# Optimization experiments

Hardware: AMD Instinct MI355X
Metric: run time of the kernel (lower is better)

The kernel has to match this reference:

```python
import jax, jax.numpy as jnp
import numpy as np

B, S, H, DH, D, FD, FU = 4, 256, 12, 64, 768, 2048, 2048


def setup_inputs() -> dict:
    key = jax.random.key(0)
    ks = jax.random.split(key, 12)
    s = 0.02  # typical init scale for weights
    return {
        "resid_pre": jax.random.normal(ks[0], (B, S, D), jnp.float32),
        "ln_scale": jax.random.uniform(ks[1], (B, S, 1), jnp.float32, 0.5, 2.0),
        "probs": jax.nn.softmax(jax.random.normal(ks[2], (B, H, S, S), jnp.float32), axis=-1),
        "W_O": jax.random.normal(ks[3], (H, DH, D), jnp.float32) * s,
        "W_V": jax.random.normal(ks[4], (H, D, DH), jnp.float32) * s,
        "enc_W": jax.random.normal(ks[5], (FD, D), jnp.float32) * s,
        "enc_b": jax.random.normal(ks[6], (FD,), jnp.float32) * s,
        "b_dec": jax.random.normal(ks[7], (D,), jnp.float32) * s,
        "up_dec_W": jax.random.normal(ks[8], (D, FU), jnp.float32) * s,
        "up_b_dec": jax.random.normal(ks[9], (D,), jnp.float32) * s,
        "pruned_features": jax.random.normal(ks[10], (B, S, FU), jnp.float32),
        "connection_mask": jax.random.randint(ks[11], (FD, FU), 0, 2, jnp.int32),
    }


def reference(resid_pre, ln_scale, probs, W_O, W_V, enc_W, enc_b, b_dec,
              up_dec_W, up_b_dec, pruned_features, connection_mask):
    # W_OV: [h, d_model(in), d_model(out)]
    W_OV = jnp.einsum('hko,hmk->hmo', W_O, W_V)
    mask = connection_mask.astype(resid_pre.dtype)

    # --- initial contributions ---
    act_ln = resid_pre / ln_scale                                  # [b,s,d]
    pre_moving = jnp.einsum('bsi,hio,fo->bshf', act_ln, W_OV, enc_W)  # [b,s,h,f_down]
    approx = jnp.einsum('bhqk,bkhf->bqf', probs, pre_moving)       # [b,q,f_down]

    # --- pruned contributions (one upstream AE) ---
    virtual = jnp.einsum('fo,hio,iu->hfu', enc_W, W_OV, up_dec_W) * mask[None]
    up_ln = pruned_features / ln_scale                             # [b,k,f_up]
    post_ov = jnp.einsum('bku,hfu->bhkf', up_ln, virtual)          # [b,h,k,f_down]
    approx = approx + jnp.einsum('bhqk,bhkf->bqf', probs, post_ov)

    # --- bias terms ---
    approx = approx + enc_b[None, None] - (enc_W @ b_dec)[None, None]
    ub_ln = up_b_dec[None, None] / ln_scale                        # [b,s,d]
    ub_post = jnp.einsum('hmd,bsm->bsd', W_OV, ub_ln)              # attn path through OV
    approx = approx + jnp.einsum('fd,bsd->bsf', enc_W, ub_post)
    return approx
```

## Files before the change

### kernel.cpp

```cpp
#include <hip/hip_runtime.h>
#include <hip/hip_bf16.h>
#include <stdint.h>

typedef __bf16 bf16;
typedef __bf16 bf16x8 __attribute__((ext_vector_type(8)));
typedef __bf16 bf16x4 __attribute__((ext_vector_type(4)));
typedef float f32x4 __attribute__((ext_vector_type(4)));

#define AS1 __attribute__((address_space(1)))
#define AS3 __attribute__((address_space(3)))


__device__ __forceinline__ void gld16(const bf16* g, bf16* l) {
  __builtin_amdgcn_global_load_lds((AS1 void*)g, (AS3 void*)l, 16, 0, 0);
}

__global__ void k_sentinel(float* __restrict__ out) {
  int i = blockIdx.x * 256 + threadIdx.x;
  if (i < 2097152) out[i] = 1048576.0f;
}


__global__ void k_invln(const float* __restrict__ ln, float* __restrict__ invln) {
  int i = blockIdx.x * 256 + threadIdx.x;
  if (i < 1024) invln[i] = 1.0f / ln[i];
}

__global__ void k_cast4(const float* __restrict__ s, bf16* __restrict__ d, int n4) {
  int i = blockIdx.x * 256 + threadIdx.x;
  if (i < n4) {
    float4 v = *(const float4*)(s + (long)i * 4);
    bf16x4 o;
    o[0] = (bf16)v.x; o[1] = (bf16)v.y; o[2] = (bf16)v.z; o[3] = (bf16)v.w;
    *(bf16x4*)(d + (long)i * 4) = o;
  }
}

__global__ void k_maskb(const int* __restrict__ m, bf16* __restrict__ d, int n4) {
  int i = blockIdx.x * 256 + threadIdx.x;
  if (i < n4) {
    int4 v = *(const int4*)(m + (long)i * 4);
    bf16x4 o;
    o[0] = (bf16)(float)v.x; o[1] = (bf16)(float)v.y;
    o[2] = (bf16)(float)v.z; o[3] = (bf16)(float)v.w;
    *(bf16x4*)(d + (long)i * 4) = o;
  }
}

__global__ void k_probsT(const float* __restrict__ probs, bf16* __restrict__ pT) {
  int i = blockIdx.x * 256 + threadIdx.x;
  if (i < 786432) {
    long idx = (long)i * 4;
    int s  = (int)(idx & 255);
    int q  = (int)((idx >> 8) & 255);
    int hb = (int)(idx >> 16);
    int h = hb % 12, b = hb / 12;
    float4 v = *(const float4*)(probs + idx);
    bf16x4 o;
    o[0] = (bf16)v.x; o[1] = (bf16)v.y; o[2] = (bf16)v.z; o[3] = (bf16)v.w;
    *(bf16x4*)(pT + (long)b * 786432 + (long)q * 3072 + h * 256 + s) = o;
  }
}

__global__ void k_WO(const float* __restrict__ W_O, bf16* __restrict__ WOb) {
  int i = blockIdx.x * 256 + threadIdx.x;
  int o = i % 768, r = (i / 768) & 127, h = i / (768 * 128);
  WOb[i] = (r < 64) ? (bf16)W_O[(long)(h * 64 + r) * 768 + o] : (bf16)0.0f;
}

__global__ void k_WVtT(const float* __restrict__ wv, bf16* __restrict__ WVt) {
  __shared__ float tile[32][33];
  int h = blockIdx.z;
  int k0 = blockIdx.x * 32;
  int i0 = blockIdx.y * 32;
  int lane = threadIdx.x & 31, rg = threadIdx.x >> 5;
  if (k0 < 64) {
    for (int r = rg; r < 32; r += 8)
      tile[r][lane] = wv[((long)(h * 768 + i0 + r)) * 64 + k0 + lane];
    __syncthreads();
    for (int r = rg; r < 32; r += 8)
      WVt[((long)h * 128 + k0 + r) * 768 + i0 + lane] = (bf16)tile[lane][r];
  } else {
    for (int r = rg; r < 32; r += 8)
      WVt[((long)h * 128 + k0 + r) * 768 + i0 + lane] = (bf16)0.0f;
  }
}

__global__ void k_WOt(const float* __restrict__ wo, bf16* __restrict__ W_Ot) {
  __shared__ float tile[32][33];
  int h = blockIdx.z;
  int k0 = blockIdx.x * 32;
  int o0 = blockIdx.y * 32;
  int lane = threadIdx.x & 31, rg = threadIdx.x >> 5;
  for (int r = rg; r < 32; r += 8)
    tile[r][lane] = wo[((long)(h * 64 + k0 + r)) * 768 + o0 + lane];
  __syncthreads();
  for (int r = rg; r < 32; r += 8)
    W_Ot[((long)(h * 768 + o0 + r)) * 64 + k0 + lane] = (bf16)tile[lane][r];
}

__global__ void k_updWtT(const float* __restrict__ u, bf16* __restrict__ d) {
  __shared__ float tile[32][33];
  int u0 = blockIdx.x * 32;
  int i0 = blockIdx.y * 32;
  int lane = threadIdx.x & 31, rg = threadIdx.x >> 5;
  for (int r = rg; r < 32; r += 8)
    tile[r][lane] = u[((long)(i0 + r)) * 2048 + u0 + lane];
  __syncthreads();
  for (int r = rg; r < 32; r += 8)
    d[((long)(u0 + r)) * 768 + i0 + lane] = (bf16)tile[lane][r];
}

__global__ void k_Xb(const float* __restrict__ resid, const float* __restrict__ invln,
                     bf16* __restrict__ Xb) {
  int i = blockIdx.x * 256 + threadIdx.x;
  if (i < 196608) {
    long idx = (long)i * 4;
    float il = invln[idx / 768];
    float4 v = *(const float4*)(resid + idx);
    bf16x4 o;
    o[0] = (bf16)(v.x * il); o[1] = (bf16)(v.y * il);
    o[2] = (bf16)(v.z * il); o[3] = (bf16)(v.w * il);
    *(bf16x4*)(Xb + idx) = o;
  }
}

__global__ void k_UtT(const float* __restrict__ pr, const float* __restrict__ invln,
                      bf16* __restrict__ Ut) {
  __shared__ float tile[32][33];
  int b = blockIdx.z, u0 = blockIdx.x * 32, s0 = blockIdx.y * 32;
  int lane = threadIdx.x & 31, rg = threadIdx.x >> 5;
  for (int r = rg; r < 32; r += 8) {
    int s = s0 + r;
    tile[r][lane] = pr[((long)(b * 256 + s)) * 2048 + u0 + lane] * invln[b * 256 + s];
  }
  __syncthreads();
  for (int r = rg; r < 32; r += 8)
    Ut[((long)b * 2048 + u0 + r) * 256 + s0 + lane] = (bf16)tile[lane][r];
}

__global__ void k_append(const bf16* __restrict__ encWb, bf16* __restrict__ Bt, long ldb) {
  int i = blockIdx.x * 256 + threadIdx.x;
  if (i < 196608) {
    long idx = (long)i * 8;
    int f = (int)(idx / 768), d = (int)(idx % 768);
    *(bf16x8*)(Bt + (long)f * ldb + d) = *(const bf16x8*)(encWb + idx);
  }
}


__device__ __forceinline__ float blk_reduce(float s) {
  __shared__ float red[256];
  red[threadIdx.x] = s; __syncthreads();
  for (int o = 128; o > 0; o >>= 1) {
    if ((int)threadIdx.x < o) red[threadIdx.x] += red[threadIdx.x + o];
    __syncthreads();
  }
  float r = red[0]; __syncthreads();
  return r;
}

__global__ void k_bias_t(const float* __restrict__ W_V, const float* __restrict__ up_b,
                         float* __restrict__ t_hk) {
  int j = blockIdx.x, h = j >> 6, k = j & 63;
  float s = 0.f;
  for (int m = threadIdx.x; m < 768; m += 256)
    s += W_V[((long)(h * 768 + m)) * 64 + k] * up_b[m];
  float r = blk_reduce(s);
  if (threadIdx.x == 0) t_hk[j] = r;
}

__global__ void k_bias_w(const float* __restrict__ W_O, const float* __restrict__ t_hk,
                         float* __restrict__ w) {
  int d = blockIdx.x;
  float s = 0.f;
  for (int j = threadIdx.x; j < 768; j += 256)
    s += W_O[(long)j * 768 + d] * t_hk[j];
  float r = blk_reduce(s);
  if (threadIdx.x == 0) w[d] = r;
}

__global__ void k_bias_c(const float* __restrict__ enc_W, const float* __restrict__ enc_b,
                         const float* __restrict__ b_dec, const float* __restrict__ w,
                         float* __restrict__ c0, float* __restrict__ c1) {
  int f = blockIdx.x;
  float s0 = 0.f, s1 = 0.f;
  for (int d = threadIdx.x; d < 768; d += 256) {
    float e = enc_W[(long)f * 768 + d];
    s0 += e * b_dec[d];
    s1 += e * w[d];
  }
  float r0 = blk_reduce(s0);
  float r1 = blk_reduce(s1);
  if (threadIdx.x == 0) { c0[f] = enc_b[f] - r0; c1[f] = r1; }
}

__global__ __launch_bounds__(256)
void gemm_bt(const bf16* __restrict__ A, const bf16* __restrict__ B, void* __restrict__ Cv,
             int M, int N, int K,
             long lda, long ldb, long ldc,
             int batchH,
             long sa_b, long sa_h, long sb_b, long sb_h, long sc_b, long sc_h,
             int mode, int kChunk,
             const bf16* __restrict__ mask, long mask_ld)
{
  __shared__ __align__(16) bf16 Asm[128 * 64];
  __shared__ __align__(16) bf16 Bsm[128 * 64];

  const int t = threadIdx.x;

  const int nbx = gridDim.x, nby = gridDim.y;
  const int nxy = nbx * nby;
  int orig = blockIdx.x + nbx * blockIdx.y;
  int qq = nxy >> 3, rr = nxy & 7;
  int xcd = orig & 7, lid = orig >> 3;
  int swz = (xcd < rr) ? (xcd * (qq + 1) + lid)
                       : (rr * (qq + 1) + (xcd - rr) * qq + lid);
  const int m0 = (swz % nby) * 128;
  const int n0 = (swz / nby) * 128;

  long aoff, boff, coff;
  int k0, k1;
  if (mode >= 2) {
    int z = blockIdx.z;
    aoff = 0; boff = 0;
    coff = (long)z * (long)M * ldc;
    k0 = z * kChunk; k1 = k0 + kChunk; if (k1 > K) k1 = K;
  } else {
    int z = blockIdx.z;
    int bb = z / batchH, hh = z - bb * batchH;
    aoff = (long)bb * sa_b + (long)hh * sa_h;
    boff = (long)bb * sb_b + (long)hh * sb_h;
    coff = (long)bb * sc_b + (long)hh * sc_h;
    k0 = 0; k1 = K;
  }

  const bf16* Ab = A + aoff + (long)m0 * lda;
  const bf16* Bb = B + boff + (long)n0 * ldb;

  const int r0 = t >> 3;
  const int g8 = t & 7;

  const int L = t & 63, w = t >> 6;
  const int wm = (w & 1) * 64, wn = (w >> 1) * 64;
  const int r16 = L & 15, q = L >> 4;

  f32x4 acc[4][4];
#pragma unroll
  for (int i = 0; i < 4; i++)
#pragma unroll
    for (int j = 0; j < 4; j++) acc[i][j] = (f32x4){0.f, 0.f, 0.f, 0.f};

  for (int kt = k0; kt < k1; kt += 64) {
#pragma unroll
    for (int j = 0; j < 4; j++) {
      int row = j * 32 + r0;
      int sc = ((g8 ^ (row & 7)) << 3);
      gld16(Ab + (long)row * lda + (kt + sc), &Asm[j * 2048 + t * 8]);
      gld16(Bb + (long)row * ldb + (kt + sc), &Bsm[j * 2048 + t * 8]);
    }
    __syncthreads();

#pragma unroll
    for (int h2 = 0; h2 < 2; h2++) {
      bf16x8 af[4], bfr[4];
#pragma unroll
      for (int i = 0; i < 4; i++) {
        int ra = wm + i * 16 + r16;
        af[i]  = *(const bf16x8*)&Asm[ra * 64 + ((((h2 << 2) + q) ^ (ra & 7)) << 3)];
        int rb = wn + i * 16 + r16;
        bfr[i] = *(const bf16x8*)&Bsm[rb * 64 + ((((h2 << 2) + q) ^ (rb & 7)) << 3)];
      }
#pragma unroll
      for (int mi = 0; mi < 4; mi++)
#pragma unroll
        for (int ni = 0; ni < 4; ni++)
          acc[mi][ni] = __builtin_amdgcn_mfma_f32_16x16x32_bf16(af[mi], bfr[ni], acc[mi][ni], 0, 0, 0);
    }
    __syncthreads();
  }

  if (mode >= 2) {
    float* C = (float*)Cv;
#pragma unroll
    for (int mi = 0; mi < 4; mi++)
#pragma unroll
      for (int ni = 0; ni < 4; ni++)
#pragma unroll
        for (int r = 0; r < 4; r++) {
          int gm = m0 + wm + mi * 16 + q * 4 + r;
          int gn = n0 + wn + ni * 16 + r16;
          long idx = coff + (long)gm * ldc + gn;
          float v = acc[mi][ni][r];
          if (mode == 3) v += C[idx];
          C[idx] = v;
        }
  } else {
    bf16* C = (bf16*)Cv;
#pragma unroll
    for (int mi = 0; mi < 4; mi++)
#pragma unroll
      for (int ni = 0; ni < 4; ni++)
#pragma unroll
        for (int r = 0; r < 4; r++) {
          int gm = m0 + wm + mi * 16 + q * 4 + r;
          int gn = n0 + wn + ni * 16 + r16;
          float v = acc[mi][ni][r];
          if (mode == 1) v *= (float)mask[(long)gm * mask_ld + gn];
          C[coff + (long)gm * ldc + gn] = (bf16)v;
        }
  }
}

__global__ __launch_bounds__(512, 2)
void gemm_fp2(const bf16* __restrict__ A, const bf16* __restrict__ B,
              float* __restrict__ C,
              int M, int N, int K, long lda, long ldb, long ldc,
              int mode, int kChunk)
{
  __shared__ __align__(16) bf16 SM[2][2][16384];

  const int t = threadIdx.x;

  const int nz = gridDim.z;
  int fid = blockIdx.x + gridDim.x * (blockIdx.y + gridDim.y * blockIdx.z);
  const int z  = fid % nz;
  const int t2 = fid / nz;
  const int m0 = (t2 >> 3) * 256;
  const int n0 = (t2 & 7) * 256;

  const long coff = (long)z * (long)M * ldc;
  int k0 = z * kChunk, k1 = k0 + kChunk; if (k1 > K) k1 = K;
  const int NT = (k1 > k0) ? (k1 - k0) >> 6 : 0;

  const bf16* Ab = A + (long)m0 * lda + k0;
  const bf16* Bb = B + (long)n0 * ldb + k0;

  const int sr = t >> 3;
  const int g8 = t & 7;

  const int L = t & 63, w = t >> 6;
  const int wm = (w & 1) * 128;
  const int wn = (w >> 1) * 64;
  const int r16 = L & 15, q = L >> 4;

  f32x4 acc[8][4];
#pragma unroll
  for (int i = 0; i < 8; i++)
#pragma unroll
    for (int j = 0; j < 4; j++) acc[i][j] = (f32x4){0.f, 0.f, 0.f, 0.f};

  auto stage = [&](int tt, int buf) {
    const bf16* Ap = Ab + (long)tt * 64;
    const bf16* Bp = Bb + (long)tt * 64;
#pragma unroll
    for (int j = 0; j < 4; j++) {
      int row = j * 64 + sr;
      int sc = ((g8 ^ (row & 7)) << 3);
      gld16(Ap + (long)row * lda + sc, &SM[buf][0][j * 4096 + t * 8]);
    }
#pragma unroll
    for (int j = 0; j < 4; j++) {
      int row = j * 64 + sr;
      int sc = ((g8 ^ (row & 7)) << 3);
      gld16(Bp + (long)row * ldb + sc, &SM[buf][1][j * 4096 + t * 8]);
    }
  };

  if (NT >= 1) stage(0, 0);

  for (int tt = 0; tt < NT; tt++) {
    if (tt + 1 < NT) {
      stage(tt + 1, (tt + 1) & 1);
      asm volatile("s_waitcnt vmcnt(8)" ::: "memory");
    } else {
      asm volatile("s_waitcnt vmcnt(0)" ::: "memory");
    }
    __builtin_amdgcn_s_barrier();

    const bf16* As = &SM[tt & 1][0][0];
    const bf16* Bs = &SM[tt & 1][1][0];
#pragma unroll
    for (int h2 = 0; h2 < 2; h2++) {
      bf16x8 af[8], bfr[4];
#pragma unroll
      for (int i = 0; i < 8; i++) {
        int ra = wm + i * 16 + r16;
        af[i]  = *(const bf16x8*)&As[ra * 64 + ((((h2 << 2) + q) ^ (ra & 7)) << 3)];
      }
#pragma unroll
      for (int i = 0; i < 4; i++) {
        int rb = wn + i * 16 + r16;
        bfr[i] = *(const bf16x8*)&Bs[rb * 64 + ((((h2 << 2) + q) ^ (rb & 7)) << 3)];
      }
#pragma unroll
      for (int mi = 0; mi < 8; mi++)
#pragma unroll
        for (int ni = 0; ni < 4; ni++)
          acc[mi][ni] = __builtin_amdgcn_mfma_f32_16x16x32_bf16(af[mi], bfr[ni], acc[mi][ni], 0, 0, 0);
    }
    __builtin_amdgcn_s_barrier();
  }

#pragma unroll
  for (int mi = 0; mi < 8; mi++)
#pragma unroll
    for (int ni = 0; ni < 4; ni++)
#pragma unroll
      for (int r = 0; r < 4; r++) {
        int gm = m0 + wm + mi * 16 + q * 4 + r;
        int gn = n0 + wn + ni * 16 + r16;
        long idx = coff + (long)gm * ldc + gn;
        float v = acc[mi][ni][r];
        if (mode == 3) v += C[idx];
        C[idx] = v;
      }
}

__global__ void k_out(const float* __restrict__ Cp, const float* __restrict__ c0,
                      const float* __restrict__ c1, const float* __restrict__ invln,
                      float* __restrict__ out, int nsplit) {
  int i4 = blockIdx.x * 256 + threadIdx.x;
  long i = (long)i4 * 4;
  int n = (int)(i & 2047), m = (int)(i >> 11);
  float4 v = *(const float4*)(Cp + i);
  for (int z = 1; z < nsplit; z++) {
    float4 u = *(const float4*)(Cp + i + (long)z * 2097152);
    v.x += u.x; v.y += u.y; v.z += u.z; v.w += u.w;
  }
  float il = invln[m];
  float4 a = *(const float4*)(c0 + n);
  float4 b = *(const float4*)(c1 + n);
  v.x += a.x + b.x * il;
  v.y += a.y + b.y * il;
  v.z += a.z + b.z * il;
  v.w += a.w + b.w * il;
  *(float4*)(out + i) = v;
}


extern "C" void kernel_launch(void* const* d_in, const int* in_sizes, int n_in,
                              void* d_out, int out_size, void* d_ws, size_t ws_size,
                              hipStream_t stream) {
  (void)out_size;
  float* out = (float*)d_out;

  int iresid = -1, iln = -1, iprobs = -1, iencb = -1, ipruned = -1, imask = -1;
  int iwo = -1, iwv = -1, iencw = -1, iupdw = -1, ibdec = -1, iupb = -1;
  for (int i = 0; i < n_in; i++) {
    switch (in_sizes[i]) {
      case 786432:  iresid  = i; break;
      case 1024:    iln     = i; break;
      case 3145728: iprobs  = i; break;
      case 2048:    iencb   = i; break;
      case 2097152: ipruned = i; break;
      case 4194304: imask   = i; break;
      case 589824:  if (iwo   < 0) iwo   = i; else iwv   = i; break;
      case 1572864: if (iencw < 0) iencw = i; else iupdw = i; break;
      case 768:     if (ibdec < 0) ibdec = i; else iupb  = i; break;
      default: break;
    }
  }
  bool ok = n_in == 12 && iresid >= 0 && iln >= 0 && iprobs >= 0 && iencb >= 0 &&
            ipruned >= 0 && imask >= 0 && iwo >= 0 && iwv >= 0 && iencw >= 0 &&
            iupdw >= 0 && ibdec >= 0 && iupb >= 0;
  if (!ok) { k_sentinel<<<8192, 256, 0, stream>>>(out); return; }

  const float* resid = (const float*)d_in[iresid];
  const float* lns   = (const float*)d_in[iln];
  const float* probs = (const float*)d_in[iprobs];
  const float* W_O   = (const float*)d_in[iwo];
  const float* W_V   = (const float*)d_in[iwv];
  const float* enc_W = (const float*)d_in[iencw];
  const float* enc_b = (const float*)d_in[iencb];
  const float* b_dec = (const float*)d_in[ibdec];
  const float* updW  = (const float*)d_in[iupdw];
  const float* up_b  = (const float*)d_in[iupb];
  const float* pruned= (const float*)d_in[ipruned];
  const int*   cmask = (const int*)d_in[imask];

  auto pad = [](size_t b) -> size_t { return (b + 255) & ~(size_t)255; };
  const size_t prepB = pad(2359296) + pad(2359296) + pad(3145728) + pad(1572864) +
                       pad(3145728) + pad(1179648) + pad(3145728) + pad(18874368);
  const size_t persB = pad(6291456) + pad(4194304) + pad(6291456) + pad(6291456) +
                       pad(8388608) + pad(4096) + pad(3072) + pad(3072) +
                       pad(8192) + pad(8192);
  auto needB = [&](int g, int ns) -> size_t {
    size_t cp = (size_t)ns * 8388608;
    size_t ov = prepB > cp ? prepB : cp;
    long KA = (long)g * 2048 + 768;
    size_t ab = pad((size_t)1024 * KA * 2) + pad((size_t)2048 * KA * 2);
    return ov + persB + ab + (2ull << 20);
  };
  const int cgs[14] = {12, 12, 12, 6, 6, 4, 3, 2, 2, 1, 1, 1, 1, 1};
  const int cns[14] = { 8,  4, 2, 8, 4, 4, 4, 4, 2, 8, 4, 2, 2, 1};
  int gs = 0, nsplit = 0;
  for (int ci = 0; ci < 14; ci++) {
    if (needB(cgs[ci], cns[ci]) <= ws_size) { gs = cgs[ci]; nsplit = cns[ci]; break; }
  }
  if (gs == 0) { gs = 1; nsplit = 1; }

  const long KA = (long)gs * 2048 + 768;

  char* p = (char*)d_ws;
  auto alloc = [&](size_t bytes) -> char* {
    char* r = p; p += (bytes + 255) & ~(size_t)255; return r;
  };
  char* overlayBase = p;
  bf16*  WOb    = (bf16*)alloc(12ull * 128 * 768 * 2);
  bf16*  WVt    = (bf16*)alloc(12ull * 128 * 768 * 2);
  bf16*  updWt  = (bf16*)alloc(2048ull * 768 * 2);
  bf16*  Xb     = (bf16*)alloc(1024ull * 768 * 2);
  bf16*  encWb  = (bf16*)alloc(2048ull * 768 * 2);
  bf16*  W_Ot   = (bf16*)alloc(12ull * 768 * 64 * 2);
  bf16*  T1     = (bf16*)alloc(12ull * 1024 * 128 * 2);
  bf16*  T3     = (bf16*)alloc(4ull * 768 * 3072 * 2);
  {
    size_t used = (size_t)(p - overlayBase);
    size_t cp = (size_t)nsplit * 8388608;
    p = overlayBase + (used > cp ? used : cp);
  }
  float* Cpart  = (float*)overlayBase;
  bf16*  G_t    = (bf16*)alloc(12ull * 2048 * 128 * 2);
  bf16*  Ut     = (bf16*)alloc(4ull * 2048 * 256 * 2);
  bf16*  E1     = (bf16*)alloc(12ull * 2048 * 128 * 2);
  bf16*  probsT = (bf16*)alloc(4ull * 256 * 3072 * 2);
  bf16*  maskb  = (bf16*)alloc(2048ull * 2048 * 2);
  float* invln  = (float*)alloc(1024 * 4);
  float* t_hk   = (float*)alloc(768 * 4);
  float* wv     = (float*)alloc(768 * 4);
  float* c0     = (float*)alloc(2048 * 4);
  float* c1     = (float*)alloc(2048 * 4);
  bf16*  A_g    = (bf16*)alloc((size_t)1024 * KA * 2);
  bf16*  B_g    = (bf16*)alloc((size_t)2048 * KA * 2);

  k_invln<<<4, 256, 0, stream>>>(lns, invln);
  k_cast4<<<1536, 256, 0, stream>>>(enc_W, encWb, 393216);
  k_probsT<<<3072, 256, 0, stream>>>(probs, probsT);
  k_maskb<<<4096, 256, 0, stream>>>(cmask, maskb, 1048576);
  k_WO<<<4608, 256, 0, stream>>>(W_O, WOb);
  k_WVtT<<<dim3(4, 24, 12), 256, 0, stream>>>(W_V, WVt);
  k_WOt<<<dim3(2, 24, 12), 256, 0, stream>>>(W_O, W_Ot);
  k_updWtT<<<dim3(64, 24), 256, 0, stream>>>(updW, updWt);
  k_Xb<<<768, 256, 0, stream>>>(resid, invln, Xb);
  k_UtT<<<dim3(64, 8, 4), 256, 0, stream>>>(pruned, invln, Ut);
  k_bias_t<<<768, 256, 0, stream>>>(W_V, up_b, t_hk);
  k_bias_w<<<768, 256, 0, stream>>>(W_O, t_hk, wv);
  k_bias_c<<<2048, 256, 0, stream>>>(enc_W, enc_b, b_dec, wv, c0, c1);

  gemm_bt<<<dim3(1, 16, 24), 256, 0, stream>>>(
      encWb, WOb, E1, 2048, 128, 768,
      768, 768, 128, 12,
      (long)(updWt - encWb), 0,
      (long)(WVt - WOb), (long)128 * 768,
      (long)(G_t - E1), (long)2048 * 128,
      0, 0, nullptr, 0);

  gemm_bt<<<dim3(1, 8, 12), 256, 0, stream>>>(
      Xb, WVt, T1, 1024, 128, 768,
      768, 768, 128, 12,
      0, 0, 0, (long)128 * 768, 0, (long)1024 * 128,
      0, 0, nullptr, 0);

  gemm_bt<<<dim3(2, 6, 48), 256, 0, stream>>>(
      W_Ot, T1, T3, 768, 256, 64,
      64, 128, 3072, 12,
      0, (long)768 * 64, (long)256 * 128, (long)1024 * 128, 2359296, 256,
      0, 0, nullptr, 0);

  gemm_bt<<<dim3(6, 2, 4), 256, 0, stream>>>(
      probsT, T3, A_g + (long)gs * 2048, 256, 768, 3072,
      3072, 3072, KA, 1,
      786432, 0, 2359296, 0, 256 * KA, 0,
      0, 0, nullptr, 0);

  k_append<<<768, 256, 0, stream>>>(encWb, B_g + (long)gs * 2048, KA);

  for (int g = 0; g < 12 / gs; g++) {
    gemm_bt<<<dim3(16, 16, gs), 256, 0, stream>>>(
        E1 + (long)g * gs * 2048 * 128, G_t + (long)g * gs * 2048 * 128, B_g,
        2048, 2048, 128,
        128, 128, KA, gs,
        0, (long)2048 * 128, 0, (long)2048 * 128, 0, 2048,
        1, 0, maskb, 2048);

    gemm_bt<<<dim3(16, 2, 4 * gs), 256, 0, stream>>>(
        probsT + (long)g * gs * 256, Ut, A_g,
        256, 2048, 256,
        3072, 256, KA, gs,
        786432, 256, (long)2048 * 256, 0, 256 * KA, 2048,
        0, 0, nullptr, 0);

    int Kthis = (g == 0) ? (int)KA : gs * 2048;
    int kc = ((Kthis / nsplit + 63) / 64) * 64;
    gemm_fp2<<<dim3(8, 4, nsplit), 512, 0, stream>>>(
        A_g, B_g, Cpart,
        1024, 2048, Kthis,
        KA, KA, 2048,
        (g == 0) ? 2 : 3, kc);
  }

  k_out<<<2048, 256, 0, stream>>>(Cpart, c0, c1, invln, out, nsplit);
}
```

Baseline: 493.1 us.

## Split-K the probs×T3 GEMM with a reduce kernel and halve virtual-weight GEMM depth

```diff
diff --git a/kernel.cpp b/kernel.cpp
--- a/kernel.cpp
+++ b/kernel.cpp
@@ -148,6 +148,23 @@
   }
 }
 
+__global__ void k_sred(const float* __restrict__ Sp, bf16* __restrict__ dst, long ldd) {
+  int i = blockIdx.x * 256 + threadIdx.x;
+  if (i < 196608) {
+    long idx = (long)i * 4;
+    int m = (int)(idx / 768), o = (int)(idx % 768);
+    float4 v = *(const float4*)(Sp + idx);
+    float4 a = *(const float4*)(Sp + 786432 + idx);
+    float4 b = *(const float4*)(Sp + 2 * 786432 + idx);
+    float4 c = *(const float4*)(Sp + 3 * 786432 + idx);
+    v.x += a.x + b.x + c.x; v.y += a.y + b.y + c.y;
+    v.z += a.z + b.z + c.z; v.w += a.w + b.w + c.w;
+    bf16x4 ov;
+    ov[0] = (bf16)v.x; ov[1] = (bf16)v.y; ov[2] = (bf16)v.z; ov[3] = (bf16)v.w;
+    *(bf16x4*)(dst + (long)m * ldd + o) = ov;
+  }
+}
+
 
 __device__ __forceinline__ float blk_reduce(float s) {
   __shared__ float red[256];
@@ -221,7 +238,14 @@
 
   long aoff, boff, coff;
   int k0, k1;
-  if (mode >= 2) {
+  if (mode == 4) {
+    int z = blockIdx.z;
+    int bb = z / batchH, kc = z - bb * batchH;
+    aoff = (long)bb * sa_b;
+    boff = (long)bb * sb_b;
+    coff = (long)bb * sc_b + (long)kc * sc_h;
+    k0 = kc * kChunk; k1 = k0 + kChunk; if (k1 > K) k1 = K;
+  } else if (mode >= 2) {
     int z = blockIdx.z;
     aoff = 0; boff = 0;
     coff = (long)z * (long)M * ldc;
@@ -481,7 +505,8 @@
 
   auto pad = [](size_t b) -> size_t { return (b + 255) & ~(size_t)255; };
   const size_t prepB = pad(2359296) + pad(2359296) + pad(3145728) + pad(1572864) +
-                       pad(3145728) + pad(1179648) + pad(3145728) + pad(18874368);
+                       pad(3145728) + pad(1179648) + pad(3145728) + pad(18874368) +
+                       pad(12582912);
   const size_t persB = pad(6291456) + pad(4194304) + pad(6291456) + pad(6291456) +
                        pad(8388608) + pad(4096) + pad(3072) + pad(3072) +
                        pad(8192) + pad(8192);
@@ -515,6 +540,7 @@
   bf16*  W_Ot   = (bf16*)alloc(12ull * 768 * 64 * 2);
   bf16*  T1     = (bf16*)alloc(12ull * 1024 * 128 * 2);
   bf16*  T3     = (bf16*)alloc(4ull * 768 * 3072 * 2);
+  float* Sp     = (float*)alloc(4ull * 1024 * 768 * 4);
   {
     size_t used = (size_t)(p - overlayBase);
     size_t cp = (size_t)nsplit * 8388608;
@@ -568,18 +594,20 @@
       0, (long)768 * 64, (long)256 * 128, (long)1024 * 128, 2359296, 256,
       0, 0, nullptr, 0);
 
-  gemm_bt<<<dim3(6, 2, 4), 256, 0, stream>>>(
-      probsT, T3, A_g + (long)gs * 2048, 256, 768, 3072,
-      3072, 3072, KA, 1,
-      786432, 0, 2359296, 0, 256 * KA, 0,
-      0, 0, nullptr, 0);
+  gemm_bt<<<dim3(6, 2, 16), 256, 0, stream>>>(
+      probsT, T3, Sp, 256, 768, 3072,
+      3072, 3072, 768, 4,
+      786432, 0, 2359296, 0, 196608, 786432,
+      4, 768, nullptr, 0);
+
+  k_sred<<<768, 256, 0, stream>>>(Sp, A_g + (long)gs * 2048, KA);
 
   k_append<<<768, 256, 0, stream>>>(encWb, B_g + (long)gs * 2048, KA);
 
   for (int g = 0; g < 12 / gs; g++) {
     gemm_bt<<<dim3(16, 16, gs), 256, 0, stream>>>(
         E1 + (long)g * gs * 2048 * 128, G_t + (long)g * gs * 2048 * 128, B_g,
-        2048, 2048, 128,
+        2048, 2048, 64,
         128, 128, KA, gs,
         0, (long)2048 * 128, 0, (long)2048 * 128, 0, 2048,
         1, 0, maskb, 2048);
```

Result: faster. 450.6 us (-8.6%).
